# Kernel optimization log

Measured on AMD Instinct MI355X. Metric: run time of the kernel, lower is better.

## Reference

```python
import jax, jax.numpy as jnp
import numpy as np

B, S, HID = 2, 2048, 2048
H, KV, D = 32, 4, 128
G = H // KV
EPS = 1e-6
SCALE = D ** -0.5
ROPE_THETA = 1000000.0


def setup_inputs() -> dict:
    key = jax.random.key(0)
    ks = jax.random.split(key, 6)
    hidden_states = jax.random.normal(ks[0], (B, S, HID), jnp.float32)
    # real RoPE tables (position_embeddings passed into forward)
    inv_freq = 1.0 / (ROPE_THETA ** (np.arange(0, D, 2, dtype=np.float32) / D))
    ang = np.arange(S, dtype=np.float32)[:, None] * inv_freq[None, :]  # [S, D/2]
    emb = np.concatenate([ang, ang], axis=-1)  # [S, D]
    cos = jnp.broadcast_to(jnp.asarray(np.cos(emb)), (B, S, D))
    sin = jnp.broadcast_to(jnp.asarray(np.sin(emb)), (B, S, D))
    sd = 0.02
    wq = jax.random.normal(ks[1], (H * D, HID), jnp.float32) * sd
    wk = jax.random.normal(ks[2], (KV * D, HID), jnp.float32) * sd
    wv = jax.random.normal(ks[3], (KV * D, HID), jnp.float32) * sd
    wo = jax.random.normal(ks[4], (HID, H * D), jnp.float32) * sd
    q_norm_w = jnp.ones((D,), jnp.float32)
    k_norm_w = jnp.ones((D,), jnp.float32)
    return {"hidden_states": hidden_states, "cos": cos, "sin": sin,
            "wq": wq, "wk": wk, "wv": wv, "wo": wo,
            "q_norm_w": q_norm_w, "k_norm_w": k_norm_w}


def _rms_norm(x, w):
    var = jnp.mean(jnp.square(x), axis=-1, keepdims=True)
    return x * jax.lax.rsqrt(var + EPS) * w


def _rotate_half(x):
    x1, x2 = jnp.split(x, 2, axis=-1)
    return jnp.concatenate([-x2, x1], axis=-1)


def _rope(x, cos, sin):
    # x: [B,S,N,D]; cos/sin: [B,S,1,D] (unsqueeze_dim=2)
    return x * cos + _rotate_half(x) * sin


def reference(hidden_states, cos, sin, wq, wk, wv, wo, q_norm_w, k_norm_w):
    x = hidden_states
    q = jnp.einsum('bsh,oh->bso', x, wq).reshape(B, S, H, D)
    k = jnp.einsum('bsh,oh->bso', x, wk).reshape(B, S, KV, D)
    v = jnp.einsum('bsh,oh->bso', x, wv).reshape(B, S, KV, D)
    q = _rms_norm(q, q_norm_w)
    k = _rms_norm(k, k_norm_w)
    c = cos[:, :, None, :]
    s = sin[:, :, None, :]
    q = _rope(q, c, s)
    k = _rope(k, c, s)
    # GQA causal attention, BSND layout
    qg = q.reshape(B, S, KV, G, D)
    scores = jnp.einsum('bqkgd,bskd->bkgqs', qg, k) * SCALE  # [B,KV,G,Sq,Sk]
    causal = jnp.tril(jnp.ones((S, S), bool))
    scores = jnp.where(causal, scores, jnp.finfo(scores.dtype).min)
    p = jax.nn.softmax(scores, axis=-1)
    out = jnp.einsum('bkgqs,bskd->bqkgd', p, v).reshape(B, S, H * D)
    return jnp.einsum('bso,ho->bsh', out, wo)
```

## Files before the change

kernel.cpp:

```cpp
#include <hip/hip_runtime.h>
#include <hip/hip_bf16.h>

typedef __attribute__((ext_vector_type(8))) short short8;
typedef __attribute__((ext_vector_type(4))) float f32x4;

#define DEVI static __device__ __forceinline__

constexpr int Bb = 2, Ss = 2048, Hh = 32, KVc = 4, Dc = 128;
constexpr float EPSc = 1e-6f;
constexpr float SCALEc = 0.08838834764831845f;

DEVI float bf2f(short s) {
  unsigned u = ((unsigned)(unsigned short)s) << 16;
  float f; __builtin_memcpy(&f, &u, 4); return f;
}
DEVI short f2bf(float f) {
  __hip_bfloat16 h = __float2bfloat16(f);
  unsigned short u; __builtin_memcpy(&u, &h, 2); return (short)u;
}

#define GLDS(gsrc, ldst) __builtin_amdgcn_global_load_lds( \
    (const __attribute__((address_space(1))) void*)(gsrc), \
    (__attribute__((address_space(3))) void*)(ldst), 16, 0, 0)

__global__ void cvt_kernel(const float* __restrict__ in, short* __restrict__ out, int n4) {
  int i = blockIdx.x * blockDim.x + threadIdx.x;
  if (i < n4) {
    float4 v = ((const float4*)in)[i];
    short4 o;
    o.x = f2bf(v.x); o.y = f2bf(v.y); o.z = f2bf(v.z); o.w = f2bf(v.w);
    ((short4*)out)[i] = o;
  }
}

template<int MODE>
__launch_bounds__(256, 2)
__global__ void gemm_bt(const short* __restrict__ A,
                        const short* __restrict__ B0,
                        const short* __restrict__ B1,
                        const short* __restrict__ B2,
                        short* __restrict__ oq,
                        short* __restrict__ ok,
                        short* __restrict__ ov,
                        float* __restrict__ of,
                        int K)
{
  __shared__ short lA[128 * 32];
  __shared__ short lB[128 * 32];
  const int tid = threadIdx.x;
  const int lane = tid & 63;
  const int wvi = tid >> 6;
  const int l15 = lane & 15, g = lane >> 4;
  const int bid = blockIdx.x;
  const int xcd = bid & 7, idx = bid >> 3;
  const int nt = (MODE == 0) ? (xcd * 5 + (idx >> 5)) : (xcd * 2 + (idx >> 5));
  const int m0 = (idx & 31) * 128;
  const short* Bp; int n0, region;
  if (MODE == 0) {
    if (nt < 32)      { Bp = B0; n0 = nt * 128;        region = 0; }
    else if (nt < 36) { Bp = B1; n0 = (nt - 32) * 128; region = 1; }
    else              { Bp = B2; n0 = (nt - 36) * 128; region = 2; }
  } else { Bp = B0; n0 = nt * 128; region = 3; }

  const int wm = (wvi >> 1) * 64, wn = (wvi & 1) * 64;
  const int srow = tid >> 2, schunk = tid & 3;

  f32x4 acc[4][4] = {};

  for (int k0 = 0; k0 < K; k0 += 32) {
    __syncthreads();
#pragma unroll
    for (int c = 0; c < 2; ++c) {
      int row = c * 64 + srow;
      int gc = schunk ^ ((row >> 1) & 3);
      GLDS(A  + (size_t)(m0 + row) * K + k0 + gc * 8, lA + (c * 256 + tid) * 8);
      GLDS(Bp + (size_t)(n0 + row) * K + k0 + gc * 8, lB + (c * 256 + tid) * 8);
    }
    __syncthreads();
    short8 afr[4], bfr[4];
#pragma unroll
    for (int i = 0; i < 4; ++i) {
      int ra = wm + i * 16 + l15;
      afr[i] = *(const short8*)(lA + ra * 32 + ((g ^ ((ra >> 1) & 3)) * 8));
      int rb = wn + i * 16 + l15;
      bfr[i] = *(const short8*)(lB + rb * 32 + ((g ^ ((rb >> 1) & 3)) * 8));
    }
#pragma unroll
    for (int mi = 0; mi < 4; ++mi)
#pragma unroll
      for (int ni = 0; ni < 4; ++ni)
        acc[mi][ni] = __builtin_amdgcn_mfma_f32_16x16x32_bf16(afr[mi], bfr[ni], acc[mi][ni], 0, 0, 0);
  }

#pragma unroll
  for (int mi = 0; mi < 4; ++mi)
#pragma unroll
    for (int ni = 0; ni < 4; ++ni)
#pragma unroll
      for (int r = 0; r < 4; ++r) {
        int m = m0 + wm + mi * 16 + g * 4 + r;
        int n = n0 + wn + ni * 16 + l15;
        float v = acc[mi][ni][r];
        if (MODE == 1) {
          of[(size_t)m * 2048 + n] = v;
        } else if (region == 0) {
          oq[(size_t)m * 4096 + n] = f2bf(v);
        } else {
          int b = m >> 11, s = m & 2047, kvi = n >> 7, d = n & 127;
          if (region == 1)
            ok[(((size_t)b * KVc + kvi) * Ss + s) * 128 + d] = f2bf(v);
          else
            ov[(((size_t)b * KVc + kvi) * 128 + d) * Ss + s] = f2bf(v);
        }
      }
}

template<bool ISQ>
__global__ void rmsnorm_rope(short* __restrict__ buf, const float* __restrict__ w,
                             const float* __restrict__ cosb, const float* __restrict__ sinb)
{
  const int lane = threadIdx.x & 63;
  const int wvi = threadIdx.x >> 6;
  const int i = blockIdx.x * 4 + wvi;
  short* row;
  int b, s;
  if (ISQ) {
    int m = i >> 5, h = i & 31;
    b = m >> 11; s = m & 2047;
    row = buf + (size_t)m * 4096 + h * 128;
  } else {
    s = i & 2047; int bkv = i >> 11; b = bkv >> 2;
    row = buf + (size_t)i * 128;
  }
  float x1 = bf2f(row[lane]), x2 = bf2f(row[lane + 64]);
  float ss = x1 * x1 + x2 * x2;
#pragma unroll
  for (int o = 32; o; o >>= 1) ss += __shfl_xor(ss, o);
  float inv = rsqrtf(ss * (1.0f / 128.0f) + EPSc);
  const float* cp = cosb + ((size_t)b * Ss + s) * Dc;
  const float* sp = sinb + ((size_t)b * Ss + s) * Dc;
  float n1 = x1 * inv * w[lane], n2 = x2 * inv * w[lane + 64];
  float o1 = n1 * cp[lane]      - n2 * sp[lane];
  float o2 = n2 * cp[lane + 64] + n1 * sp[lane + 64];
  if (ISQ) { o1 *= SCALEc; o2 *= SCALEc; }
  row[lane]      = f2bf(o1);
  row[lane + 64] = f2bf(o2);
}

__launch_bounds__(256, 2)
__global__ void attn_fwd(const short* __restrict__ qb,
                         const short* __restrict__ kbuf,
                         const short* __restrict__ vtbuf,
                         short* __restrict__ ob)
{
  __shared__ short lK[2][64 * 128];
  __shared__ short lV[2][128 * 64];
  __shared__ short lP[4][32 * 32];
  const int tid = threadIdx.x, lane = tid & 63, wvi = tid >> 6;
  const int l15 = lane & 15, g = lane >> 4;
  const int pi = blockIdx.x, h = blockIdx.y, b = blockIdx.z;
  const int kv = h >> 3;
  const short* kp = kbuf  + ((size_t)b * KVc + kv) * Ss * 128;
  const short* vp = vtbuf + ((size_t)b * KVc + kv) * 128 * Ss;
  const int krow = tid >> 4, kch = tid & 15;
  const int vrow = tid >> 3, vch = tid & 7;

  for (int which = 0; which < 2; ++which) {
    const int qt = which ? (15 - pi) : pi;
    const int qwb = qt * 128 + wvi * 32;
    const int nkt = 2 * qt + 2;

    short8 qf[2][4];
#pragma unroll
    for (int qs = 0; qs < 2; ++qs)
#pragma unroll
      for (int dc = 0; dc < 4; ++dc)
        qf[qs][dc] = *(const short8*)(qb + (size_t)(b * Ss + qwb + qs * 16 + l15) * 4096
                                         + h * 128 + dc * 32 + g * 8);

    f32x4 oacc[2][8] = {};
    float mrun[2] = { -__builtin_inff(), -__builtin_inff() };
    float lrun[2] = { 0.f, 0.f };

    auto STAGE = [&](int kt, int bufi) {
      const int kb0 = kt * 64;
#pragma unroll
      for (int c = 0; c < 4; ++c) {
        int r = c * 16 + krow;
        int gc = kch ^ (r & 7);
        GLDS(kp + (size_t)(kb0 + r) * 128 + gc * 8, &lK[bufi][(c * 256 + tid) * 8]);
      }
#pragma unroll
      for (int c = 0; c < 4; ++c) {
        int r = c * 32 + vrow;
        int gc = vch ^ (r & 7);
        GLDS(vp + (size_t)r * Ss + kb0 + gc * 8, &lV[bufi][(c * 256 + tid) * 8]);
      }
    };

    STAGE(0, 0);
    STAGE(1, 1);

    for (int kt = 0; kt < nkt; ++kt) {
      const int cb = kt & 1;
      if (kt + 1 < nkt) asm volatile("s_waitcnt vmcnt(8)" ::: "memory");
      else              asm volatile("s_waitcnt vmcnt(0)" ::: "memory");
      __builtin_amdgcn_s_barrier();
      asm volatile("" ::: "memory");

#pragma unroll
      for (int half = 0; half < 2; ++half) {
        const int kb0 = kt * 64 + half * 32;
        if (kb0 <= qwb + 31) {
          short8 kf[2][4];
#pragma unroll
          for (int ks = 0; ks < 2; ++ks)
#pragma unroll
            for (int dc = 0; dc < 4; ++dc) {
              int row = half * 32 + ks * 16 + l15;
              kf[ks][dc] = *(const short8*)(&lK[cb][0] + row * 128 + (((dc * 4 + g) ^ (row & 7)) * 8));
            }
          f32x4 st[2][2] = {};
          __builtin_amdgcn_s_setprio(1);
#pragma unroll
          for (int qs = 0; qs < 2; ++qs)
#pragma unroll
            for (int ks = 0; ks < 2; ++ks)
#pragma unroll
              for (int dc = 0; dc < 4; ++dc)
                st[qs][ks] = __builtin_amdgcn_mfma_f32_16x16x32_bf16(kf[ks][dc], qf[qs][dc], st[qs][ks], 0, 0, 0);
          __builtin_amdgcn_s_setprio(0);

          const bool need_mask = (kb0 + 31 > qwb);
#pragma unroll
          for (int qs = 0; qs < 2; ++qs) {
            const int qg = qwb + qs * 16 + l15;
            float p[8];
            float tmax = -__builtin_inff();
#pragma unroll
            for (int ks = 0; ks < 2; ++ks)
#pragma unroll
              for (int r = 0; r < 4; ++r) {
                float v = st[qs][ks][r];
                if (need_mask && (kb0 + ks * 16 + g * 4 + r > qg)) v = -__builtin_inff();
                p[ks * 4 + r] = v;
                tmax = fmaxf(tmax, v);
              }
            tmax = fmaxf(tmax, __shfl_xor(tmax, 16));
            tmax = fmaxf(tmax, __shfl_xor(tmax, 32));
            float m_use = mrun[qs];
            if (__any(tmax > m_use + 8.0f)) {
              float mnew = fmaxf(m_use, tmax);
              float scl = __expf(m_use - mnew);
              lrun[qs] *= scl;
              mrun[qs] = mnew;
#pragma unroll
              for (int r = 0; r < 4; ++r) {
                float sc = __shfl(scl, g * 4 + r);
#pragma unroll
                for (int dt = 0; dt < 8; ++dt)
                  oacc[qs][dt][r] *= sc;
              }
              m_use = mnew;
            }
            float rsum = 0.f;
#pragma unroll
            for (int j = 0; j < 8; ++j) { p[j] = __expf(p[j] - m_use); rsum += p[j]; }
            rsum += __shfl_xor(rsum, 16);
            rsum += __shfl_xor(rsum, 32);
            lrun[qs] += rsum;
            {
              int row = qs * 16 + l15;
              int sw = (row >> 1) & 3;
              short* pr = lP[wvi] + row * 32;
#pragma unroll
              for (int ks = 0; ks < 2; ++ks) {
                int idx = (((2 * ks + (g >> 1)) ^ sw) * 8) + (g & 1) * 4;
                short4 pw;
                pw.x = f2bf(p[ks * 4 + 0]);
                pw.y = f2bf(p[ks * 4 + 1]);
                pw.z = f2bf(p[ks * 4 + 2]);
                pw.w = f2bf(p[ks * 4 + 3]);
                *(short4*)(pr + idx) = pw;
              }
            }
          }
          asm volatile("" ::: "memory");
          short8 vf[8];
#pragma unroll
          for (int dt = 0; dt < 8; ++dt) {
            int row = dt * 16 + l15;
            vf[dt] = *(const short8*)(&lV[cb][0] + row * 64 + (((half * 4 + g) ^ (row & 7)) * 8));
          }
          __builtin_amdgcn_s_setprio(1);
#pragma unroll
          for (int qs = 0; qs < 2; ++qs) {
            int row = qs * 16 + l15;
            short8 pf = *(const short8*)(lP[wvi] + row * 32 + ((g ^ ((row >> 1) & 3)) * 8));
#pragma unroll
            for (int dt = 0; dt < 8; ++dt)
              oacc[qs][dt] = __builtin_amdgcn_mfma_f32_16x16x32_bf16(pf, vf[dt], oacc[qs][dt], 0, 0, 0);
          }
          __builtin_amdgcn_s_setprio(0);
          asm volatile("" ::: "memory");
        }
      }

      asm volatile("" ::: "memory");
      __builtin_amdgcn_s_barrier();
      if (kt + 2 < nkt) STAGE(kt + 2, cb);
    }

#pragma unroll
    for (int qs = 0; qs < 2; ++qs)
#pragma unroll
      for (int r = 0; r < 4; ++r) {
        float inv = 1.0f / __shfl(lrun[qs], g * 4 + r);
        int qrow = qwb + qs * 16 + g * 4 + r;
        short* op = ob + (size_t)(b * Ss + qrow) * 4096 + h * 128;
#pragma unroll
        for (int dt = 0; dt < 8; ++dt)
          op[dt * 16 + l15] = f2bf(oacc[qs][dt][r] * inv);
      }
  }
}

extern "C" void kernel_launch(void* const* d_in, const int* in_sizes, int n_in,
                              void* d_out, int out_size, void* d_ws, size_t ws_size,
                              hipStream_t stream) {
  const float* x    = (const float*)d_in[0];
  const float* cosb = (const float*)d_in[1];
  const float* sinb = (const float*)d_in[2];
  const float* wq   = (const float*)d_in[3];
  const float* wk   = (const float*)d_in[4];
  const float* wv   = (const float*)d_in[5];
  const float* wo   = (const float*)d_in[6];
  const float* qw   = (const float*)d_in[7];
  const float* kw   = (const float*)d_in[8];

  size_t off = 0;
  auto alloc = [&](size_t bytes) {
    char* p = (char*)d_ws + off;
    off += (bytes + 255) & ~(size_t)255;
    return p;
  };
  short* x_bf  = (short*)alloc((size_t)8388608 * 2);
  short* wq_bf = (short*)alloc((size_t)8388608 * 2);
  short* wk_bf = (short*)alloc((size_t)1048576 * 2);
  short* wv_bf = (short*)alloc((size_t)1048576 * 2);
  short* wo_bf = (short*)alloc((size_t)8388608 * 2);
  short* q_bf  = (short*)alloc((size_t)16777216 * 2);
  short* k_bf  = (short*)alloc((size_t)2097152 * 2);
  short* v_bf  = (short*)alloc((size_t)2097152 * 2);
  short* ao_bf = (short*)alloc((size_t)16777216 * 2);

  auto cv = [&](const float* s, short* d, int n) {
    int n4 = n / 4;
    cvt_kernel<<<(n4 + 255) / 256, 256, 0, stream>>>(s, d, n4);
  };
  cv(x,  x_bf,  8388608);
  cv(wq, wq_bf, 8388608);
  cv(wk, wk_bf, 1048576);
  cv(wv, wv_bf, 1048576);
  cv(wo, wo_bf, 8388608);

  gemm_bt<0><<<1280, 256, 0, stream>>>(x_bf, wq_bf, wk_bf, wv_bf,
                                       q_bf, k_bf, v_bf, nullptr, 2048);
  rmsnorm_rope<true><<<32768, 256, 0, stream>>>(q_bf, qw, cosb, sinb);
  rmsnorm_rope<false><<<4096, 256, 0, stream>>>(k_bf, kw, cosb, sinb);
  attn_fwd<<<dim3(8, 32, 2), 256, 0, stream>>>(q_bf, k_bf, v_bf, ao_bf);
  gemm_bt<1><<<512, 256, 0, stream>>>(ao_bf, wo_bf, nullptr, nullptr,
                                      nullptr, nullptr, nullptr, (float*)d_out, 4096);
}
```

Baseline: 385.2 us.

## Fuse RMSNorm+RoPE into QKV GEMM epilogue and merge conversion launches

Removes the two separate rmsnorm_rope kernels. Each GEMM wave now owns full 128-wide rows (32x128 per wave instead of 64x64), so the per-head RMS reduction can run in the epilogue with shuffles, followed by RoPE before the bf16 store. The five fp32->bf16 conversion launches become one grid-stride kernel. The XCD-aware block remapping is dropped in favour of a plain 2D grid, which may hurt L2 locality. The new wave tiling also loads 8 B fragments and only 2 A fragments per wave, which changes LDS traffic.

```diff
diff --git a/kernel.cpp b/kernel.cpp
--- a/kernel.cpp
+++ b/kernel.cpp
@@ -23,13 +23,19 @@
     (const __attribute__((address_space(1))) void*)(gsrc), \
     (__attribute__((address_space(3))) void*)(ldst), 16, 0, 0)
 
-__global__ void cvt_kernel(const float* __restrict__ in, short* __restrict__ out, int n4) {
-  int i = blockIdx.x * blockDim.x + threadIdx.x;
-  if (i < n4) {
-    float4 v = ((const float4*)in)[i];
+struct Cvt5 { const float* src[5]; short* dst[5]; };
+__global__ void cvt_all(Cvt5 a) {
+  constexpr int CUM[6] = {0, 2097152, 4194304, 4456448, 4718592, 6815744};
+  const int stride = gridDim.x * blockDim.x;
+  for (int i = blockIdx.x * blockDim.x + threadIdx.x; i < 6815744; i += stride) {
+    int s = 0;
+#pragma unroll
+    for (int t = 1; t < 5; ++t) if (i >= CUM[t]) s = t;
+    int j = i - CUM[s];
+    float4 v = ((const float4*)a.src[s])[j];
     short4 o;
     o.x = f2bf(v.x); o.y = f2bf(v.y); o.z = f2bf(v.z); o.w = f2bf(v.w);
-    ((short4*)out)[i] = o;
+    ((short4*)a.dst[s])[j] = o;
   }
 }
 
@@ -43,6 +49,10 @@
                         short* __restrict__ ok,
                         short* __restrict__ ov,
                         float* __restrict__ of,
+                        const float* __restrict__ cosb,
+                        const float* __restrict__ sinb,
+                        const float* __restrict__ qnw,
+                        const float* __restrict__ knw,
                         int K)
 {
   __shared__ short lA[128 * 32];
@@ -51,10 +61,8 @@
   const int lane = tid & 63;
   const int wvi = tid >> 6;
   const int l15 = lane & 15, g = lane >> 4;
-  const int bid = blockIdx.x;
-  const int xcd = bid & 7, idx = bid >> 3;
-  const int nt = (MODE == 0) ? (xcd * 5 + (idx >> 5)) : (xcd * 2 + (idx >> 5));
-  const int m0 = (idx & 31) * 128;
+  const int m0 = blockIdx.x * 128;
+  const int nt = blockIdx.y;
   const short* Bp; int n0, region;
   if (MODE == 0) {
     if (nt < 32)      { Bp = B0; n0 = nt * 128;        region = 0; }
@@ -62,10 +70,10 @@
     else              { Bp = B2; n0 = (nt - 36) * 128; region = 2; }
   } else { Bp = B0; n0 = nt * 128; region = 3; }
 
-  const int wm = (wvi >> 1) * 64, wn = (wvi & 1) * 64;
+  const int wrow = wvi * 32;
   const int srow = tid >> 2, schunk = tid & 3;
 
-  f32x4 acc[4][4] = {};
+  f32x4 acc[2][8] = {};
 
   for (int k0 = 0; k0 < K; k0 += 32) {
     __syncthreads();
@@ -77,74 +85,89 @@
       GLDS(Bp + (size_t)(n0 + row) * K + k0 + gc * 8, lB + (c * 256 + tid) * 8);
     }
     __syncthreads();
-    short8 afr[4], bfr[4];
-#pragma unroll
-    for (int i = 0; i < 4; ++i) {
-      int ra = wm + i * 16 + l15;
+    short8 afr[2], bfr[8];
+#pragma unroll
+    for (int i = 0; i < 2; ++i) {
+      int ra = wrow + i * 16 + l15;
       afr[i] = *(const short8*)(lA + ra * 32 + ((g ^ ((ra >> 1) & 3)) * 8));
-      int rb = wn + i * 16 + l15;
+    }
+#pragma unroll
+    for (int i = 0; i < 8; ++i) {
+      int rb = i * 16 + l15;
       bfr[i] = *(const short8*)(lB + rb * 32 + ((g ^ ((rb >> 1) & 3)) * 8));
     }
 #pragma unroll
-    for (int mi = 0; mi < 4; ++mi)
-#pragma unroll
-      for (int ni = 0; ni < 4; ++ni)
+    for (int mi = 0; mi < 2; ++mi)
+#pragma unroll
+      for (int ni = 0; ni < 8; ++ni)
         acc[mi][ni] = __builtin_amdgcn_mfma_f32_16x16x32_bf16(afr[mi], bfr[ni], acc[mi][ni], 0, 0, 0);
   }
 
-#pragma unroll
-  for (int mi = 0; mi < 4; ++mi)
-#pragma unroll
-    for (int ni = 0; ni < 4; ++ni)
+  if (MODE == 1) {
+#pragma unroll
+    for (int mi = 0; mi < 2; ++mi)
 #pragma unroll
       for (int r = 0; r < 4; ++r) {
-        int m = m0 + wm + mi * 16 + g * 4 + r;
-        int n = n0 + wn + ni * 16 + l15;
-        float v = acc[mi][ni][r];
-        if (MODE == 1) {
-          of[(size_t)m * 2048 + n] = v;
-        } else if (region == 0) {
-          oq[(size_t)m * 4096 + n] = f2bf(v);
-        } else {
-          int b = m >> 11, s = m & 2047, kvi = n >> 7, d = n & 127;
-          if (region == 1)
-            ok[(((size_t)b * KVc + kvi) * Ss + s) * 128 + d] = f2bf(v);
-          else
-            ov[(((size_t)b * KVc + kvi) * 128 + d) * Ss + s] = f2bf(v);
+        int m = m0 + wrow + mi * 16 + g * 4 + r;
+#pragma unroll
+        for (int ni = 0; ni < 8; ++ni)
+          of[(size_t)m * 2048 + n0 + ni * 16 + l15] = acc[mi][ni][r];
+      }
+  } else if (region == 2) {
+#pragma unroll
+    for (int mi = 0; mi < 2; ++mi)
+#pragma unroll
+      for (int r = 0; r < 4; ++r) {
+        int m = m0 + wrow + mi * 16 + g * 4 + r;
+        int b = m >> 11, s = m & 2047;
+#pragma unroll
+        for (int ni = 0; ni < 8; ++ni) {
+          int n = n0 + ni * 16 + l15;
+          int kvi = n >> 7, d = n & 127;
+          ov[(((size_t)b * KVc + kvi) * 128 + d) * Ss + s] = f2bf(acc[mi][ni][r]);
         }
       }
-}
-
-template<bool ISQ>
-__global__ void rmsnorm_rope(short* __restrict__ buf, const float* __restrict__ w,
-                             const float* __restrict__ cosb, const float* __restrict__ sinb)
-{
-  const int lane = threadIdx.x & 63;
-  const int wvi = threadIdx.x >> 6;
-  const int i = blockIdx.x * 4 + wvi;
-  short* row;
-  int b, s;
-  if (ISQ) {
-    int m = i >> 5, h = i & 31;
-    b = m >> 11; s = m & 2047;
-    row = buf + (size_t)m * 4096 + h * 128;
   } else {
-    s = i & 2047; int bkv = i >> 11; b = bkv >> 2;
-    row = buf + (size_t)i * 128;
+    const float* wnorm = (region == 0) ? qnw : knw;
+    float w8[8];
+#pragma unroll
+    for (int ni = 0; ni < 8; ++ni) w8[ni] = wnorm[ni * 16 + l15];
+#pragma unroll
+    for (int mi = 0; mi < 2; ++mi)
+#pragma unroll
+      for (int r = 0; r < 4; ++r) {
+        int m = m0 + wrow + mi * 16 + g * 4 + r;
+        int b = m >> 11, s = m & 2047;
+        float xv[8];
+        float ssq = 0.f;
+#pragma unroll
+        for (int ni = 0; ni < 8; ++ni) { xv[ni] = acc[mi][ni][r]; ssq += xv[ni] * xv[ni]; }
+        ssq += __shfl_xor(ssq, 1);
+        ssq += __shfl_xor(ssq, 2);
+        ssq += __shfl_xor(ssq, 4);
+        ssq += __shfl_xor(ssq, 8);
+        float inv = rsqrtf(ssq * (1.0f / 128.0f) + EPSc);
+        float xn[8];
+#pragma unroll
+        for (int ni = 0; ni < 8; ++ni) xn[ni] = xv[ni] * inv * w8[ni];
+        const float* cpr = cosb + ((size_t)b * Ss + s) * Dc;
+        const float* spr = sinb + ((size_t)b * Ss + s) * Dc;
+#pragma unroll
+        for (int ni = 0; ni < 8; ++ni) {
+          int dl = ni * 16 + l15;
+          float c = cpr[dl], sn = spr[dl];
+          float rot = (ni < 4) ? -xn[ni + 4] : xn[ni - 4];
+          float o = xn[ni] * c + rot * sn;
+          int n = n0 + dl;
+          if (region == 0) {
+            oq[(size_t)m * 4096 + n] = f2bf(o * SCALEc);
+          } else {
+            int kvi = n >> 7, d = n & 127;
+            ok[(((size_t)b * KVc + kvi) * Ss + s) * 128 + d] = f2bf(o);
+          }
+        }
+      }
   }
-  float x1 = bf2f(row[lane]), x2 = bf2f(row[lane + 64]);
-  float ss = x1 * x1 + x2 * x2;
-#pragma unroll
-  for (int o = 32; o; o >>= 1) ss += __shfl_xor(ss, o);
-  float inv = rsqrtf(ss * (1.0f / 128.0f) + EPSc);
-  const float* cp = cosb + ((size_t)b * Ss + s) * Dc;
-  const float* sp = sinb + ((size_t)b * Ss + s) * Dc;
-  float n1 = x1 * inv * w[lane], n2 = x2 * inv * w[lane + 64];
-  float o1 = n1 * cp[lane]      - n2 * sp[lane];
-  float o2 = n2 * cp[lane + 64] + n1 * sp[lane + 64];
-  if (ISQ) { o1 *= SCALEc; o2 *= SCALEc; }
-  row[lane]      = f2bf(o1);
-  row[lane + 64] = f2bf(o2);
 }
 
 __launch_bounds__(256, 2)
@@ -354,21 +377,19 @@
   short* v_bf  = (short*)alloc((size_t)2097152 * 2);
   short* ao_bf = (short*)alloc((size_t)16777216 * 2);
 
-  auto cv = [&](const float* s, short* d, int n) {
-    int n4 = n / 4;
-    cvt_kernel<<<(n4 + 255) / 256, 256, 0, stream>>>(s, d, n4);
-  };
-  cv(x,  x_bf,  8388608);
-  cv(wq, wq_bf, 8388608);
-  cv(wk, wk_bf, 1048576);
-  cv(wv, wv_bf, 1048576);
-  cv(wo, wo_bf, 8388608);
-
-  gemm_bt<0><<<1280, 256, 0, stream>>>(x_bf, wq_bf, wk_bf, wv_bf,
-                                       q_bf, k_bf, v_bf, nullptr, 2048);
-  rmsnorm_rope<true><<<32768, 256, 0, stream>>>(q_bf, qw, cosb, sinb);
-  rmsnorm_rope<false><<<4096, 256, 0, stream>>>(k_bf, kw, cosb, sinb);
+  Cvt5 ca;
+  ca.src[0] = x;    ca.dst[0] = x_bf;
+  ca.src[1] = wq;   ca.dst[1] = wq_bf;
+  ca.src[2] = wk;   ca.dst[2] = wk_bf;
+  ca.src[3] = wv;   ca.dst[3] = wv_bf;
+  ca.src[4] = wo;   ca.dst[4] = wo_bf;
+  cvt_all<<<2048, 256, 0, stream>>>(ca);
+
+  gemm_bt<0><<<dim3(32, 40), 256, 0, stream>>>(x_bf, wq_bf, wk_bf, wv_bf,
+                                               q_bf, k_bf, v_bf, nullptr,
+                                               cosb, sinb, qw, kw, 2048);
   attn_fwd<<<dim3(8, 32, 2), 256, 0, stream>>>(q_bf, k_bf, v_bf, ao_bf);
-  gemm_bt<1><<<512, 256, 0, stream>>>(ao_bf, wo_bf, nullptr, nullptr,
-                                      nullptr, nullptr, nullptr, (float*)d_out, 4096);
-}
+  gemm_bt<1><<<dim3(32, 16), 256, 0, stream>>>(ao_bf, wo_bf, nullptr, nullptr,
+                                               nullptr, nullptr, nullptr, (float*)d_out,
+                                               nullptr, nullptr, nullptr, nullptr, 4096);
+}
```

New measurement: 355.0 us. 7.9% less time.
